# Kernel optimization log

Hardware: AMD Instinct MI355X
Metric: run time of the kernel (lower is better)

The kernel has to match this reference:

```python
import jax, jax.numpy as jnp
import numpy as np

BN_EPS = 1e-5


def setup_inputs() -> dict:
    key = jax.random.key(0)
    ks = jax.random.split(key, 4)
    S, B, F, P, T, H, W = 4, 2, 64, 16, 32, 64, 64
    HID = 32
    feats = jax.random.normal(ks[0], (S, B, F, T, H, W), dtype=jnp.float32)
    p_s = jax.random.normal(ks[1], (B, P, T, H, W), dtype=jnp.float32)
    w1 = jax.random.normal(ks[2], (HID, F + P), dtype=jnp.float32) * (1.0 / np.sqrt(F + P))
    w2 = jax.random.normal(ks[3], (HID,), dtype=jnp.float32) * (1.0 / np.sqrt(HID))
    return {
        "feats": feats,
        "p_s": p_s,
        "w1": w1,
        "bn_gamma": jnp.ones((HID,), jnp.float32),
        "bn_beta": jnp.zeros((HID,), jnp.float32),
        "bn_mean": jnp.zeros((HID,), jnp.float32),
        "bn_var": jnp.ones((HID,), jnp.float32),
        "w2": w2,
        "b2": jnp.zeros((1,), jnp.float32),
    }


def reference(feats, p_s, w1, bn_gamma, bn_beta, bn_mean, bn_var, w2, b2):
    # feats: [S,B,F,T,H,W]; p_s: [B,P,T,H,W]
    F = feats.shape[2]
    w1_f, w1_p = w1[:, :F], w1[:, F:]
    # 1x1x1 conv on concat([f, p_s]) == split contraction; avoids materializing concat
    h = jnp.einsum('of,sbfthw->sbothw', w1_f, feats) \
        + jnp.einsum('op,bpthw->bothw', w1_p, p_s)[None]
    # BatchNorm3d (inference form) folded to scale/shift, then ReLU
    scale = bn_gamma / jnp.sqrt(bn_var + BN_EPS)
    shift = bn_beta - bn_mean * scale
    h = jax.nn.relu(h * scale[:, None, None, None] + shift[:, None, None, None])
    # second 1x1x1 conv: hidden -> 1 logit per branch
    logits = jnp.einsum('sbothw,o->sbthw', h, w2) + b2[0]
    alpha = jax.nn.softmax(logits, axis=0)            # softmax over branches S
    out = jnp.einsum('sbfthw,sbthw->bfthw', feats, alpha)
    return out, jnp.moveaxis(alpha, 0, 1)             # out:[B,F,T,H,W], alpha:[B,S,T,H,W]
```

## Files before the change

### kernel.cpp

```cpp
#include <hip/hip_runtime.h>
#include <hip/hip_bf16.h>
#include <stdint.h>

#define THW   131072
#define NS    4
#define NB    2
#define NF    64
#define NP    16
#define HID   32
#define BN_EPS 1e-5f
#define PXT   128
#define TPB   4

typedef short  bf16x8  __attribute__((ext_vector_type(8)));
typedef float  f32x16  __attribute__((ext_vector_type(16)));

union FragU { uint32_t u[4]; bf16x8 v; uint4 q; };

__device__ __forceinline__ uint32_t pk2(float a, float b) {
    __hip_bfloat162 h = __float22bfloat162_rn(make_float2(a, b));
    uint32_t r;
    __builtin_memcpy(&r, &h, sizeof(r));
    return r;
}
__device__ __forceinline__ float lo16(uint32_t u) { return __builtin_bit_cast(float, u << 16); }
__device__ __forceinline__ float hi16(uint32_t u) { return __builtin_bit_cast(float, u & 0xFFFF0000u); }

__device__ __forceinline__ void glds16(const float* g, void* l) {
    __builtin_amdgcn_global_load_lds(
        (const __attribute__((address_space(1))) uint32_t*)g,
        (__attribute__((address_space(3))) uint32_t*)l, 16, 0, 0);
}

__global__ __launch_bounds__(256, 2) void gssm_kernel(
    const float* __restrict__ feats, const float* __restrict__ ps,
    const float* __restrict__ w1,    const float* __restrict__ gamma,
    const float* __restrict__ beta,  const float* __restrict__ mean,
    const float* __restrict__ var,   const float* __restrict__ w2,
    float* __restrict__ out)
{
    __shared__ __align__(16) float    fbuf[2][NF][PXT];
    __shared__ __align__(16) float    pbuf[NP][PXT];
    __shared__ __align__(16) uint32_t w1lds[32 * 44];
    __shared__ float2 tbl[HID];

    const int tid  = threadIdx.x;
    const int lane = tid & 63;
    const int wv   = tid >> 6;
    const int hi   = lane >> 5;
    const int ln   = lane & 31;

    for (int t = tid; t < 1280; t += 256) {
        float2 v = ((const float2*)w1)[t];
        int o = t / 40, cp = t - o * 40;
        float sc = gamma[o] * rsqrtf(var[o] + BN_EPS);
        w1lds[o * 44 + (cp >> 3) * 8 + (cp & 7)] = pk2(v.x * sc, v.y * sc);
    }
    if (tid < HID) {
        float sc = gamma[tid] * rsqrtf(var[tid] + BN_EPS);
        tbl[tid] = make_float2(beta[tid] - mean[tid] * sc, w2[tid]);
    }
    asm volatile("s_waitcnt vmcnt(0)" ::: "memory");

    const int base9 = (int)(__brev((unsigned)blockIdx.x) >> 23);
    const long sstr = (long)NB * NF * THW;
    const long pl_off = (long)(lane >> 5) * THW + (ln << 2);
    const int  f0     = wv * 16;

    auto tile_b   = [&](int t) { return (4 * base9 + t) >> 10; };
    auto tile_px0 = [&](int t) { return ((4 * base9 + t) * PXT) & (THW - 1); };

    auto stage_feats = [&](int t, int s, int buf) {
        const float* base = feats + (long)tile_b(t) * NF * THW + tile_px0(t)
                          + (long)s * sstr;
        #pragma unroll
        for (int i = 0; i < 8; ++i) {
            int f = f0 + i * 2;
            glds16(base + (long)f * THW + pl_off, (void*)&fbuf[buf][f][0]);
        }
    };
    auto stage_p = [&](int t) {
        const float* base = ps + (long)tile_b(t) * NP * THW + tile_px0(t);
        #pragma unroll
        for (int i = 0; i < 2; ++i) {
            int p = wv * 4 + i * 2;
            glds16(base + (long)p * THW + pl_off, (void*)&pbuf[p][0]);
        }
    };

    stage_p(0);
    stage_feats(0, 0, 0);
    asm volatile("s_waitcnt lgkmcnt(0)" ::: "memory");
    __builtin_amdgcn_s_barrier();

    FragU afr[5];
    {
        const uint32_t abase = (uint32_t)(ln * 44 + hi * 4);
        #pragma unroll
        for (int k = 0; k < 5; ++k)
            afr[k].q = *((const uint4*)&w1lds[abase + k * 8]);
    }
    float sh[16], wo[16];
    #pragma unroll
    for (int r = 0; r < 16; ++r) {
        float2 t2 = tbl[(r & 3) + 8 * (r >> 2) + 4 * hi];
        sh[r] = t2.x;
        wo[r] = t2.y;
    }

    const int pxloc = wv * 32 + ln;

    FragU bp;
    auto consume = [&](int buf, FragU* pk) -> float {
        #pragma unroll
        for (int kb = 0; kb < 4; ++kb)
            #pragma unroll
            for (int r = 0; r < 4; ++r)
                pk[kb].u[r] = pk2(fbuf[buf][kb * 16 + hi * 8 + 2 * r][pxloc],
                                  fbuf[buf][kb * 16 + hi * 8 + 2 * r + 1][pxloc]);
        f32x16 acc;
        #pragma unroll
        for (int r = 0; r < 16; ++r) acc[r] = 0.f;
        acc = __builtin_amdgcn_mfma_f32_32x32x16_bf16(afr[4].v, bp.v,    acc, 0, 0, 0);
        acc = __builtin_amdgcn_mfma_f32_32x32x16_bf16(afr[0].v, pk[0].v, acc, 0, 0, 0);
        acc = __builtin_amdgcn_mfma_f32_32x32x16_bf16(afr[1].v, pk[1].v, acc, 0, 0, 0);
        acc = __builtin_amdgcn_mfma_f32_32x32x16_bf16(afr[2].v, pk[2].v, acc, 0, 0, 0);
        acc = __builtin_amdgcn_mfma_f32_32x32x16_bf16(afr[3].v, pk[3].v, acc, 0, 0, 0);
        float pp4[4] = {0.f, 0.f, 0.f, 0.f};
        #pragma unroll
        for (int r = 0; r < 16; ++r) {
            float h = fmaxf(acc[r] + sh[r], 0.f);
            pp4[r & 3] = fmaf(h, wo[r], pp4[r & 3]);
        }
        float part = (pp4[0] + pp4[1]) + (pp4[2] + pp4[3]);
        return part + __shfl_xor(part, 32);
    };

    for (int t = 0; t < TPB; ++t) {
        FragU pk0[4], pk1[4], pk2f[4], pk3[4];
        float lg0, lg1, lg2, lg3;

        stage_feats(t, 1, 1);
        asm volatile("s_waitcnt vmcnt(8)" ::: "memory");
        __builtin_amdgcn_s_barrier();
        #pragma unroll
        for (int r = 0; r < 4; ++r)
            bp.u[r] = pk2(pbuf[hi * 8 + 2 * r][pxloc], pbuf[hi * 8 + 2 * r + 1][pxloc]);
        lg0 = consume(0, pk0);
        __builtin_amdgcn_s_barrier();

        stage_feats(t, 2, 0);
        asm volatile("s_waitcnt vmcnt(8)" ::: "memory");
        __builtin_amdgcn_s_barrier();
        lg1 = consume(1, pk1);
        __builtin_amdgcn_s_barrier();

        stage_feats(t, 3, 1);
        asm volatile("s_waitcnt vmcnt(8)" ::: "memory");
        __builtin_amdgcn_s_barrier();
        lg2 = consume(0, pk2f);
        __builtin_amdgcn_s_barrier();

        if (t + 1 < TPB) {
            stage_p(t + 1);
            stage_feats(t + 1, 0, 0);
            asm volatile("s_waitcnt vmcnt(10)" ::: "memory");
        } else {
            asm volatile("s_waitcnt vmcnt(0)" ::: "memory");
        }
        __builtin_amdgcn_s_barrier();
        lg3 = consume(1, pk3);

        const float m   = fmaxf(fmaxf(lg0, lg1), fmaxf(lg2, lg3));
        const float e0  = __expf(lg0 - m), e1 = __expf(lg1 - m);
        const float e2  = __expf(lg2 - m), e3 = __expf(lg3 - m);
        const float inv = 1.f / (e0 + e1 + e2 + e3);
        const float a0 = e0 * inv, a1 = e1 * inv, a2 = e2 * inv, a3 = e3 * inv;

        const int b   = tile_b(t);
        const int thw = tile_px0(t) + pxloc;

        float* ob = out + ((long)(b * NF + hi * 8)) * THW + thw;
        #pragma unroll
        for (int k = 0; k < 4; ++k)
            #pragma unroll
            for (int r = 0; r < 4; ++r) {
                float vlo = a0 * lo16(pk0[k].u[r]);
                float vhi = a0 * hi16(pk0[k].u[r]);
                vlo = fmaf(a1, lo16(pk1[k].u[r]), vlo);
                vhi = fmaf(a1, hi16(pk1[k].u[r]), vhi);
                vlo = fmaf(a2, lo16(pk2f[k].u[r]), vlo);
                vhi = fmaf(a2, hi16(pk2f[k].u[r]), vhi);
                vlo = fmaf(a3, lo16(pk3[k].u[r]), vlo);
                vhi = fmaf(a3, hi16(pk3[k].u[r]), vhi);
                ob[(long)(k * 16 + 2 * r)     * THW] = vlo;
                ob[(long)(k * 16 + 2 * r + 1) * THW] = vhi;
            }

        float* ab = out + (long)NB * NF * THW + ((long)(b * NS + hi * 2)) * THW + thw;
        ab[0]   = hi ? a2 : a0;
        ab[THW] = hi ? a3 : a1;

        __builtin_amdgcn_s_barrier();
    }
}

extern "C" void kernel_launch(void* const* d_in, const int* in_sizes, int n_in,
                              void* d_out, int out_size, void* d_ws, size_t ws_size,
                              hipStream_t stream) {
    const float* feats = (const float*)d_in[0];
    const float* ps    = (const float*)d_in[1];
    const float* w1    = (const float*)d_in[2];
    const float* gamma = (const float*)d_in[3];
    const float* beta  = (const float*)d_in[4];
    const float* mean  = (const float*)d_in[5];
    const float* var   = (const float*)d_in[6];
    const float* w2    = (const float*)d_in[7];
    float* out = (float*)d_out;

    dim3 grid(512), block(256);
    hipLaunchKernelGGL(gssm_kernel, grid, block, 0, stream,
                       feats, ps, w1, gamma, beta, mean, var, w2, out);
}
```

Before: 80.10 us.

## Give each wave a private LDS pixel slice and drop block barriers

Shared-memory staging buffers are split per wave, so each wave loads only the 32 pixels it consumes, with all 64 channels, into its own region. Because no wave reads another wave's staged data, every block-wide s_barrier in the tile loop is removed. Ordering now relies only on per-wave vmcnt waits, including a new count for the first stage of later tiles that allows for the previous tile's outstanding stores. This removes inter-wave stalls in a memory-bound streaming loop, at the cost of fragile hand-tuned wait counts.

```diff
diff --git a/kernel.cpp b/kernel.cpp
--- a/kernel.cpp
+++ b/kernel.cpp
@@ -10,6 +10,7 @@
 #define HID   32
 #define BN_EPS 1e-5f
 #define PXT   128
+#define PXW   32
 #define TPB   4
 
 typedef short  bf16x8  __attribute__((ext_vector_type(8)));
@@ -39,8 +40,8 @@
     const float* __restrict__ var,   const float* __restrict__ w2,
     float* __restrict__ out)
 {
-    __shared__ __align__(16) float    fbuf[2][NF][PXT];
-    __shared__ __align__(16) float    pbuf[NP][PXT];
+    __shared__ __align__(16) float    fbuf[4][2][NF][PXW];
+    __shared__ __align__(16) float    pbuf[4][NP][PXW];
     __shared__ __align__(16) uint32_t w1lds[32 * 44];
     __shared__ float2 tbl[HID];
 
@@ -64,28 +65,24 @@
 
     const int base9 = (int)(__brev((unsigned)blockIdx.x) >> 23);
     const long sstr = (long)NB * NF * THW;
-    const long pl_off = (long)(lane >> 5) * THW + (ln << 2);
-    const int  f0     = wv * 16;
+
+    const long lsub = (long)(lane >> 3) * THW + (long)(lane & 7) * 4;
 
     auto tile_b   = [&](int t) { return (4 * base9 + t) >> 10; };
     auto tile_px0 = [&](int t) { return ((4 * base9 + t) * PXT) & (THW - 1); };
 
     auto stage_feats = [&](int t, int s, int buf) {
         const float* base = feats + (long)tile_b(t) * NF * THW + tile_px0(t)
-                          + (long)s * sstr;
-        #pragma unroll
-        for (int i = 0; i < 8; ++i) {
-            int f = f0 + i * 2;
-            glds16(base + (long)f * THW + pl_off, (void*)&fbuf[buf][f][0]);
-        }
+                          + wv * PXW + (long)s * sstr;
+        #pragma unroll
+        for (int i = 0; i < 8; ++i)
+            glds16(base + (long)(i * 8) * THW + lsub, (void*)&fbuf[wv][buf][i * 8][0]);
     };
     auto stage_p = [&](int t) {
-        const float* base = ps + (long)tile_b(t) * NP * THW + tile_px0(t);
-        #pragma unroll
-        for (int i = 0; i < 2; ++i) {
-            int p = wv * 4 + i * 2;
-            glds16(base + (long)p * THW + pl_off, (void*)&pbuf[p][0]);
-        }
+        const float* base = ps + (long)tile_b(t) * NP * THW + tile_px0(t) + wv * PXW;
+        #pragma unroll
+        for (int j = 0; j < 2; ++j)
+            glds16(base + (long)(j * 8) * THW + lsub, (void*)&pbuf[wv][j * 8][0]);
     };
 
     stage_p(0);
@@ -108,16 +105,14 @@
         wo[r] = t2.y;
     }
 
-    const int pxloc = wv * 32 + ln;
-
     FragU bp;
     auto consume = [&](int buf, FragU* pk) -> float {
         #pragma unroll
         for (int kb = 0; kb < 4; ++kb)
             #pragma unroll
             for (int r = 0; r < 4; ++r)
-                pk[kb].u[r] = pk2(fbuf[buf][kb * 16 + hi * 8 + 2 * r][pxloc],
-                                  fbuf[buf][kb * 16 + hi * 8 + 2 * r + 1][pxloc]);
+                pk[kb].u[r] = pk2(fbuf[wv][buf][kb * 16 + hi * 8 + 2 * r][ln],
+                                  fbuf[wv][buf][kb * 16 + hi * 8 + 2 * r + 1][ln]);
         f32x16 acc;
         #pragma unroll
         for (int r = 0; r < 16; ++r) acc[r] = 0.f;
@@ -141,25 +136,20 @@
         float lg0, lg1, lg2, lg3;
 
         stage_feats(t, 1, 1);
-        asm volatile("s_waitcnt vmcnt(8)" ::: "memory");
-        __builtin_amdgcn_s_barrier();
+        if (t == 0) { asm volatile("s_waitcnt vmcnt(8)"  ::: "memory"); }
+        else        { asm volatile("s_waitcnt vmcnt(42)" ::: "memory"); }
         #pragma unroll
         for (int r = 0; r < 4; ++r)
-            bp.u[r] = pk2(pbuf[hi * 8 + 2 * r][pxloc], pbuf[hi * 8 + 2 * r + 1][pxloc]);
+            bp.u[r] = pk2(pbuf[wv][hi * 8 + 2 * r][ln], pbuf[wv][hi * 8 + 2 * r + 1][ln]);
         lg0 = consume(0, pk0);
-        __builtin_amdgcn_s_barrier();
 
         stage_feats(t, 2, 0);
         asm volatile("s_waitcnt vmcnt(8)" ::: "memory");
-        __builtin_amdgcn_s_barrier();
         lg1 = consume(1, pk1);
-        __builtin_amdgcn_s_barrier();
 
         stage_feats(t, 3, 1);
         asm volatile("s_waitcnt vmcnt(8)" ::: "memory");
-        __builtin_amdgcn_s_barrier();
         lg2 = consume(0, pk2f);
-        __builtin_amdgcn_s_barrier();
 
         if (t + 1 < TPB) {
             stage_p(t + 1);
@@ -168,7 +158,6 @@
         } else {
             asm volatile("s_waitcnt vmcnt(0)" ::: "memory");
         }
-        __builtin_amdgcn_s_barrier();
         lg3 = consume(1, pk3);
 
         const float m   = fmaxf(fmaxf(lg0, lg1), fmaxf(lg2, lg3));
@@ -178,7 +167,7 @@
         const float a0 = e0 * inv, a1 = e1 * inv, a2 = e2 * inv, a3 = e3 * inv;
 
         const int b   = tile_b(t);
-        const int thw = tile_px0(t) + pxloc;
+        const int thw = tile_px0(t) + wv * PXW + ln;
 
         float* ob = out + ((long)(b * NF + hi * 8)) * THW + thw;
         #pragma unroll
@@ -200,8 +189,6 @@
         float* ab = out + (long)NB * NF * THW + ((long)(b * NS + hi * 2)) * THW + thw;
         ab[0]   = hi ? a2 : a0;
         ab[THW] = hi ? a3 : a1;
-
-        __builtin_amdgcn_s_barrier();
     }
 }
 
```

Result: no change. 80.73 us (+0.8%).
